# Performance work log

Measured on AMD Instinct MI355X. Metric: run time of the kernel, lower is better.

## Reference

```python
import jax, jax.numpy as jnp
import numpy as np


def setup_inputs() -> dict:
    key = jax.random.key(0)
    inputs = jax.random.normal(key, (4, 1024, 64), dtype=jnp.float32)
    return {"inputs": inputs}


def reference(inputs):
    # inputs: (B, N, D)
    # scores[b,i,j] = sum_d tanh(x[b,i,d] + x[b,j,d])
    addition = inputs[:, :, None, :] + inputs[:, None, :, :]  # (B, N, N, D)
    e_values = jnp.tanh(addition).sum(axis=-1)                # (B, N, N)
    weights = jax.nn.softmax(e_values, axis=-1)               # (B, N, N)
    out = jnp.einsum("bij,bjd->bid", weights, inputs)         # (B, N, D)
    return out
```

## Files before the change

### kernel.cpp

```cpp
#include <hip/hip_runtime.h>


#define NB 4
#define NN 1024
#define ND 64
#define TJ 64
#define NWAVES 4
#define NTILES (NN / TJ)

#if __has_builtin(__builtin_amdgcn_exp2f)
#define EXP2F(x) __builtin_amdgcn_exp2f(x)
#else
#define EXP2F(x) exp2f(x)
#endif
#if __has_builtin(__builtin_amdgcn_rcpf)
#define RCPF(x) __builtin_amdgcn_rcpf(x)
#else
#define RCPF(x) (1.0f / (x))
#endif

static constexpr float C_SCALE = 2.8853900817779268f;

__device__ __forceinline__ float readlane_f(float v, int l) {
    return __uint_as_float(__builtin_amdgcn_readlane(__float_as_uint(v), l));
}

__global__ __launch_bounds__(256) void prep_kernel(const float* __restrict__ x,
                                                   float* __restrict__ E) {
    int idx = blockIdx.x * 256 + threadIdx.x;
    float4 v = ((const float4*)x)[idx];
    float4 e;
    e.x = EXP2F(C_SCALE * v.x);
    e.y = EXP2F(C_SCALE * v.y);
    e.z = EXP2F(C_SCALE * v.z);
    e.w = EXP2F(C_SCALE * v.w);
    ((float4*)E)[idx] = e;
}

template <bool HAS_E>
__global__ __launch_bounds__(256) void addattn_kernel(const float* __restrict__ x,
                                                      const float* __restrict__ E,
                                                      float* __restrict__ out) {
    __shared__ float x_lds[TJ * ND];
    __shared__ float E_lds[TJ * ND];
    __shared__ float Ei_lds[NWAVES * ND];

    const int tid   = threadIdx.x;
    const int lane  = tid & 63;
    const int wave  = tid >> 6;
    const int wg    = blockIdx.x;
    const int b     = wg >> 8;
    const int ibase = (wg & 255) * NWAVES;

    const float* xb = x + (size_t)b * NN * ND;
    const float* Eb = E + (size_t)b * NN * ND;

    Ei_lds[tid] = EXP2F(C_SCALE * xb[(size_t)ibase * ND + tid]);

    float acc    = 0.0f;
    float denomp = 0.0f;

    for (int t = 0; t < NTILES; ++t) {
        __syncthreads();
        {
            const float4* srcx = (const float4*)(xb + (size_t)t * TJ * ND);
            const float4* srcE = (const float4*)(Eb + (size_t)t * TJ * ND);
            #pragma unroll
            for (int it = 0; it < (TJ * ND / 4) / 256; ++it) {
                int idx = it * 256 + tid;
                int j   = idx >> 4;
                int d4  = idx & 15;
                float4 xv = srcx[idx];
                ((float4*)x_lds)[idx] = xv;
                float4 ev;
                if (HAS_E) {
                    ev = srcE[idx];
                } else {
                    ev.x = EXP2F(C_SCALE * xv.x);
                    ev.y = EXP2F(C_SCALE * xv.y);
                    ev.z = EXP2F(C_SCALE * xv.z);
                    ev.w = EXP2F(C_SCALE * xv.w);
                }
                *(float4*)&E_lds[j * ND + ((d4 ^ (j & 15)) << 2)] = ev;
            }
        }
        __syncthreads();

        const int xorkey = lane & 15;
        const float* Eirow = &Ei_lds[wave * ND];
        float rs0 = 0.f, rs1 = 0.f, rs2 = 0.f, rs3 = 0.f;
        #pragma unroll
        for (int d4 = 0; d4 < 16; ++d4) {
            float4 ej = *(const float4*)&E_lds[lane * ND + ((d4 ^ xorkey) << 2)];
            float4 ei = *(const float4*)&Eirow[d4 * 4];
            rs0 += RCPF(fmaf(ei.x, ej.x, 1.0f));
            rs1 += RCPF(fmaf(ei.y, ej.y, 1.0f));
            rs2 += RCPF(fmaf(ei.z, ej.z, 1.0f));
            rs3 += RCPF(fmaf(ei.w, ej.w, 1.0f));
        }
        float rsum = (rs0 + rs1) + (rs2 + rs3);
        float w = EXP2F(-C_SCALE * rsum);
        denomp += w;

        #pragma unroll
        for (int j = 0; j < TJ; ++j) {
            float wj = readlane_f(w, j);
            acc = fmaf(wj, x_lds[j * ND + lane], acc);
        }
    }

    #pragma unroll
    for (int s = 0; s < 6; ++s) denomp += __shfl_xor(denomp, 1 << s, 64);

    const int i = ibase + wave;
    out[((size_t)b * NN + i) * ND + lane] = acc * RCPF(denomp);
}

extern "C" void kernel_launch(void* const* d_in, const int* in_sizes, int n_in,
                              void* d_out, int out_size, void* d_ws, size_t ws_size,
                              hipStream_t stream) {
    const float* x = (const float*)d_in[0];
    float* out = (float*)d_out;
    const size_t e_bytes = (size_t)NB * NN * ND * sizeof(float);

    dim3 grid(NB * (NN / NWAVES));
    dim3 block(256);

    if (ws_size >= e_bytes) {
        float* E = (float*)d_ws;
        prep_kernel<<<dim3(NB * NN * ND / 4 / 256), dim3(256), 0, stream>>>(x, E);
        addattn_kernel<true><<<grid, block, 0, stream>>>(x, E, out);
    } else {
        addattn_kernel<false><<<grid, block, 0, stream>>>(x, (const float*)nullptr, out);
    }
}
```

Before: 74.98 us.

## Process two query rows per wave and stage softmax weights through LDS

Each wave now handles two query rows instead of one, so every key E tile and x tile read from LDS is reused twice, and the grid shrinks to 128 blocks per batch. The per-lane readlane broadcast in the weighted sum is replaced by writing weights to LDS and reading them back as float4, with split accumulators for more instruction-level parallelism. A constant shift is added to the exp2 argument to keep the weights in range. The trade-offs are more registers per thread, fewer total workgroups, and extra LDS traffic for the weights.

```diff
diff --git a/kernel.cpp b/kernel.cpp
--- a/kernel.cpp
+++ b/kernel.cpp
@@ -5,7 +5,8 @@
 #define NN 1024
 #define ND 64
 #define TJ 64
-#define NWAVES 4
+#define TI 8
+#define IPW 2
 #define NTILES (NN / TJ)
 
 #if __has_builtin(__builtin_amdgcn_exp2f)
@@ -20,10 +21,7 @@
 #endif
 
 static constexpr float C_SCALE = 2.8853900817779268f;
-
-__device__ __forceinline__ float readlane_f(float v, int l) {
-    return __uint_as_float(__builtin_amdgcn_readlane(__float_as_uint(v), l));
-}
+static constexpr float K_SHIFT = 46.166241308446828f;
 
 __global__ __launch_bounds__(256) void prep_kernel(const float* __restrict__ x,
                                                    float* __restrict__ E) {
@@ -41,24 +39,37 @@
 __global__ __launch_bounds__(256) void addattn_kernel(const float* __restrict__ x,
                                                       const float* __restrict__ E,
                                                       float* __restrict__ out) {
+    __shared__ float E_lds[TJ * ND];
     __shared__ float x_lds[TJ * ND];
-    __shared__ float E_lds[TJ * ND];
-    __shared__ float Ei_lds[NWAVES * ND];
+    __shared__ float Ei_lds[TI * ND];
+    __shared__ float w_lds[4 * IPW * ND];
 
     const int tid   = threadIdx.x;
     const int lane  = tid & 63;
     const int wave  = tid >> 6;
     const int wg    = blockIdx.x;
-    const int b     = wg >> 8;
-    const int ibase = (wg & 255) * NWAVES;
+    const int b     = wg >> 7;
+    const int ibase = (wg & 127) * TI;
 
     const float* xb = x + (size_t)b * NN * ND;
     const float* Eb = E + (size_t)b * NN * ND;
 
-    Ei_lds[tid] = EXP2F(C_SCALE * xb[(size_t)ibase * ND + tid]);
+    if (tid < TI * ND / 4) {
+        if (HAS_E) {
+            ((float4*)Ei_lds)[tid] = ((const float4*)(Eb + (size_t)ibase * ND))[tid];
+        } else {
+            float4 v = ((const float4*)(xb + (size_t)ibase * ND))[tid];
+            float4 e;
+            e.x = EXP2F(C_SCALE * v.x);
+            e.y = EXP2F(C_SCALE * v.y);
+            e.z = EXP2F(C_SCALE * v.z);
+            e.w = EXP2F(C_SCALE * v.w);
+            ((float4*)Ei_lds)[tid] = e;
+        }
+    }
 
-    float acc    = 0.0f;
-    float denomp = 0.0f;
+    float acc0a = 0.f, acc0b = 0.f, acc1a = 0.f, acc1b = 0.f;
+    float dn0 = 0.f, dn1 = 0.f;
 
     for (int t = 0; t < NTILES; ++t) {
         __syncthreads();
@@ -69,7 +80,7 @@
             for (int it = 0; it < (TJ * ND / 4) / 256; ++it) {
                 int idx = it * 256 + tid;
                 int j   = idx >> 4;
-                int d4  = idx & 15;
+                int c   = idx & 15;
                 float4 xv = srcx[idx];
                 ((float4*)x_lds)[idx] = xv;
                 float4 ev;
@@ -81,39 +92,88 @@
                     ev.z = EXP2F(C_SCALE * xv.z);
                     ev.w = EXP2F(C_SCALE * xv.w);
                 }
-                *(float4*)&E_lds[j * ND + ((d4 ^ (j & 15)) << 2)] = ev;
+                *(float4*)&E_lds[j * ND + ((c ^ (j & 15)) << 2)] = ev;
             }
         }
         __syncthreads();
 
         const int xorkey = lane & 15;
-        const float* Eirow = &Ei_lds[wave * ND];
-        float rs0 = 0.f, rs1 = 0.f, rs2 = 0.f, rs3 = 0.f;
+        const float* Ei0 = &Ei_lds[(wave * IPW + 0) * ND];
+        const float* Ei1 = &Ei_lds[(wave * IPW + 1) * ND];
+        float4 rs0 = {0.f, 0.f, 0.f, 0.f};
+        float4 rs1 = {0.f, 0.f, 0.f, 0.f};
         #pragma unroll
-        for (int d4 = 0; d4 < 16; ++d4) {
-            float4 ej = *(const float4*)&E_lds[lane * ND + ((d4 ^ xorkey) << 2)];
-            float4 ei = *(const float4*)&Eirow[d4 * 4];
-            rs0 += RCPF(fmaf(ei.x, ej.x, 1.0f));
-            rs1 += RCPF(fmaf(ei.y, ej.y, 1.0f));
-            rs2 += RCPF(fmaf(ei.z, ej.z, 1.0f));
-            rs3 += RCPF(fmaf(ei.w, ej.w, 1.0f));
+        for (int c = 0; c < 16; ++c) {
+            float4 ej = *(const float4*)&E_lds[lane * ND + ((c ^ xorkey) << 2)];
+            float4 e0 = *(const float4*)&Ei0[c * 4];
+            float4 e1 = *(const float4*)&Ei1[c * 4];
+            rs0.x += RCPF(fmaf(e0.x, ej.x, 1.0f));
+            rs0.y += RCPF(fmaf(e0.y, ej.y, 1.0f));
+            rs0.z += RCPF(fmaf(e0.z, ej.z, 1.0f));
+            rs0.w += RCPF(fmaf(e0.w, ej.w, 1.0f));
+            rs1.x += RCPF(fmaf(e1.x, ej.x, 1.0f));
+            rs1.y += RCPF(fmaf(e1.y, ej.y, 1.0f));
+            rs1.z += RCPF(fmaf(e1.z, ej.z, 1.0f));
+            rs1.w += RCPF(fmaf(e1.w, ej.w, 1.0f));
         }
-        float rsum = (rs0 + rs1) + (rs2 + rs3);
-        float w = EXP2F(-C_SCALE * rsum);
-        denomp += w;
+        float r0 = (rs0.x + rs0.y) + (rs0.z + rs0.w);
+        float r1 = (rs1.x + rs1.y) + (rs1.z + rs1.w);
+        float w0 = EXP2F(fmaf(-C_SCALE, r0, K_SHIFT));
+        float w1 = EXP2F(fmaf(-C_SCALE, r1, K_SHIFT));
+        dn0 += w0;
+        dn1 += w1;
+
+        w_lds[(wave * IPW + 0) * ND + lane] = w0;
+        w_lds[(wave * IPW + 1) * ND + lane] = w1;
 
         #pragma unroll
-        for (int j = 0; j < TJ; ++j) {
-            float wj = readlane_f(w, j);
-            acc = fmaf(wj, x_lds[j * ND + lane], acc);
+        for (int j8 = 0; j8 < 8; ++j8) {
+            {
+                const int j4 = j8 * 2;
+                float4 wq0 = *(const float4*)&w_lds[(wave * IPW + 0) * ND + j4 * 4];
+                float4 wq1 = *(const float4*)&w_lds[(wave * IPW + 1) * ND + j4 * 4];
+                float xv0 = x_lds[(j4 * 4 + 0) * ND + lane];
+                float xv1 = x_lds[(j4 * 4 + 1) * ND + lane];
+                float xv2 = x_lds[(j4 * 4 + 2) * ND + lane];
+                float xv3 = x_lds[(j4 * 4 + 3) * ND + lane];
+                acc0a = fmaf(wq0.x, xv0, acc0a);
+                acc0a = fmaf(wq0.y, xv1, acc0a);
+                acc0a = fmaf(wq0.z, xv2, acc0a);
+                acc0a = fmaf(wq0.w, xv3, acc0a);
+                acc1a = fmaf(wq1.x, xv0, acc1a);
+                acc1a = fmaf(wq1.y, xv1, acc1a);
+                acc1a = fmaf(wq1.z, xv2, acc1a);
+                acc1a = fmaf(wq1.w, xv3, acc1a);
+            }
+            {
+                const int j4 = j8 * 2 + 1;
+                float4 wq0 = *(const float4*)&w_lds[(wave * IPW + 0) * ND + j4 * 4];
+                float4 wq1 = *(const float4*)&w_lds[(wave * IPW + 1) * ND + j4 * 4];
+                float xv0 = x_lds[(j4 * 4 + 0) * ND + lane];
+                float xv1 = x_lds[(j4 * 4 + 1) * ND + lane];
+                float xv2 = x_lds[(j4 * 4 + 2) * ND + lane];
+                float xv3 = x_lds[(j4 * 4 + 3) * ND + lane];
+                acc0b = fmaf(wq0.x, xv0, acc0b);
+                acc0b = fmaf(wq0.y, xv1, acc0b);
+                acc0b = fmaf(wq0.z, xv2, acc0b);
+                acc0b = fmaf(wq0.w, xv3, acc0b);
+                acc1b = fmaf(wq1.x, xv0, acc1b);
+                acc1b = fmaf(wq1.y, xv1, acc1b);
+                acc1b = fmaf(wq1.z, xv2, acc1b);
+                acc1b = fmaf(wq1.w, xv3, acc1b);
+            }
         }
     }
 
     #pragma unroll
-    for (int s = 0; s < 6; ++s) denomp += __shfl_xor(denomp, 1 << s, 64);
+    for (int s = 0; s < 6; ++s) {
+        dn0 += __shfl_xor(dn0, 1 << s, 64);
+        dn1 += __shfl_xor(dn1, 1 << s, 64);
+    }
 
-    const int i = ibase + wave;
-    out[((size_t)b * NN + i) * ND + lane] = acc * RCPF(denomp);
+    const int i0 = ibase + wave * IPW;
+    out[((size_t)b * NN + i0) * ND + lane]     = (acc0a + acc0b) * RCPF(dn0);
+    out[((size_t)b * NN + i0 + 1) * ND + lane] = (acc1a + acc1b) * RCPF(dn1);
 }
 
 extern "C" void kernel_launch(void* const* d_in, const int* in_sizes, int n_in,
@@ -123,7 +183,7 @@
     float* out = (float*)d_out;
     const size_t e_bytes = (size_t)NB * NN * ND * sizeof(float);
 
-    dim3 grid(NB * (NN / NWAVES));
+    dim3 grid(NB * (NN / TI));
     dim3 block(256);
 
     if (ws_size >= e_bytes) {
```

Measured after the change: 70.92 us. -5.4%, faster.

## Pair tanh reciprocals algebraically and accumulate output per-lane with packed FMAs

Applied to the files above, without the earlier changes.

Combines two reciprocal terms per pair of dimensions into one rcp via the identity 1/(1+a)+1/(1+q) = (2+a+q)/(1+a+q+aq). This halves the transcendental count and uses packed v2f FMAs. The weighted sum over j becomes a per-lane accumulation of 64 output dims in registers, followed by a butterfly transpose-reduction at the end, replacing 64 readlanes per tile. It also reads Ei from global/registers instead of LDS, swizzles x_lds, adds a constant shift to the exponent, and raises the occupancy hint. The trade-offs are much higher register pressure and a costly final shuffle reduction.

```diff
diff --git a/kernel.cpp b/kernel.cpp
--- a/kernel.cpp
+++ b/kernel.cpp
@@ -5,7 +5,7 @@
 #define NN 1024
 #define ND 64
 #define TJ 64
-#define NWAVES 4
+#define TI 4
 #define NTILES (NN / TJ)
 
 #if __has_builtin(__builtin_amdgcn_exp2f)
@@ -20,10 +20,14 @@
 #endif
 
 static constexpr float C_SCALE = 2.8853900817779268f;
+static constexpr float K_SHIFT = 46.166241308446828f;
 
-__device__ __forceinline__ float readlane_f(float v, int l) {
-    return __uint_as_float(__builtin_amdgcn_readlane(__float_as_uint(v), l));
-}
+typedef float v2f __attribute__((ext_vector_type(2)));
+
+#define PKFMA(a, b, c) __builtin_elementwise_fma((a), (b), (c))
+
+__device__ __forceinline__ v2f vlo(float4 v) { v2f r; r.x = v.x; r.y = v.y; return r; }
+__device__ __forceinline__ v2f vhi(float4 v) { v2f r; r.x = v.z; r.y = v.w; return r; }
 
 __global__ __launch_bounds__(256) void prep_kernel(const float* __restrict__ x,
                                                    float* __restrict__ E) {
@@ -38,27 +42,43 @@
 }
 
 template <bool HAS_E>
-__global__ __launch_bounds__(256) void addattn_kernel(const float* __restrict__ x,
-                                                      const float* __restrict__ E,
-                                                      float* __restrict__ out) {
+__global__ __launch_bounds__(256, 3) void addattn_kernel(const float* __restrict__ x,
+                                                         const float* __restrict__ E,
+                                                         float* __restrict__ out) {
+    __shared__ float E_lds[TJ * ND];
     __shared__ float x_lds[TJ * ND];
-    __shared__ float E_lds[TJ * ND];
-    __shared__ float Ei_lds[NWAVES * ND];
 
     const int tid   = threadIdx.x;
     const int lane  = tid & 63;
     const int wave  = tid >> 6;
     const int wg    = blockIdx.x;
     const int b     = wg >> 8;
-    const int ibase = (wg & 255) * NWAVES;
+    const int ibase = (wg & 255) * TI;
+    const int i0    = __builtin_amdgcn_readfirstlane(ibase + wave);
 
-    const float* xb = x + (size_t)b * NN * ND;
-    const float* Eb = E + (size_t)b * NN * ND;
+    const float* xb  = x + (size_t)b * NN * ND;
+    const float* Eb  = E + (size_t)b * NN * ND;
+    const float* Eip = Eb + (size_t)i0 * ND;
 
-    Ei_lds[tid] = EXP2F(C_SCALE * xb[(size_t)ibase * ND + tid]);
+    v2f ei2[32];
+    if (!HAS_E) {
+        #pragma unroll
+        for (int c = 0; c < 16; ++c) {
+            float4 xiq = *(const float4*)&xb[(size_t)i0 * ND + c * 4];
+            v2f lo, hi;
+            lo.x = EXP2F(C_SCALE * xiq.x);
+            lo.y = EXP2F(C_SCALE * xiq.y);
+            hi.x = EXP2F(C_SCALE * xiq.z);
+            hi.y = EXP2F(C_SCALE * xiq.w);
+            ei2[2 * c] = lo;
+            ei2[2 * c + 1] = hi;
+        }
+    }
 
-    float acc    = 0.0f;
-    float denomp = 0.0f;
+    v2f acc2[32];
+    #pragma unroll
+    for (int k = 0; k < 32; ++k) acc2[k] = (v2f){0.f, 0.f};
+    float dn = 0.f;
 
     for (int t = 0; t < NTILES; ++t) {
         __syncthreads();
@@ -69,9 +89,10 @@
             for (int it = 0; it < (TJ * ND / 4) / 256; ++it) {
                 int idx = it * 256 + tid;
                 int j   = idx >> 4;
-                int d4  = idx & 15;
+                int c   = idx & 15;
+                int w   = j * ND + ((c ^ (j & 15)) << 2);
                 float4 xv = srcx[idx];
-                ((float4*)x_lds)[idx] = xv;
+                *(float4*)&x_lds[w] = xv;
                 float4 ev;
                 if (HAS_E) {
                     ev = srcE[idx];
@@ -81,39 +102,62 @@
                     ev.z = EXP2F(C_SCALE * xv.z);
                     ev.w = EXP2F(C_SCALE * xv.w);
                 }
-                *(float4*)&E_lds[j * ND + ((d4 ^ (j & 15)) << 2)] = ev;
+                *(float4*)&E_lds[w] = ev;
             }
         }
         __syncthreads();
 
-        const int xorkey = lane & 15;
-        const float* Eirow = &Ei_lds[wave * ND];
-        float rs0 = 0.f, rs1 = 0.f, rs2 = 0.f, rs3 = 0.f;
+        const int key = lane & 15;
+        v2f rse = {0.f, 0.f}, rso = {0.f, 0.f};
         #pragma unroll
-        for (int d4 = 0; d4 < 16; ++d4) {
-            float4 ej = *(const float4*)&E_lds[lane * ND + ((d4 ^ xorkey) << 2)];
-            float4 ei = *(const float4*)&Eirow[d4 * 4];
-            rs0 += RCPF(fmaf(ei.x, ej.x, 1.0f));
-            rs1 += RCPF(fmaf(ei.y, ej.y, 1.0f));
-            rs2 += RCPF(fmaf(ei.z, ej.z, 1.0f));
-            rs3 += RCPF(fmaf(ei.w, ej.w, 1.0f));
+        for (int c = 0; c < 16; ++c) {
+            float4 ejq = *(const float4*)&E_lds[lane * ND + ((c ^ key) << 2)];
+            v2f eil, eih;
+            if (HAS_E) {
+                float4 eiq = *(const float4*)&Eip[c * 4];
+                eil = vlo(eiq); eih = vhi(eiq);
+            } else {
+                eil = ei2[2 * c]; eih = ei2[2 * c + 1];
+            }
+            v2f a = eil * vlo(ejq);
+            v2f q = eih * vhi(ejq);
+            v2f p = a + q;
+            v2f r = PKFMA(a, q, p + 1.0f);
+            v2f tt; tt.x = RCPF(r.x); tt.y = RCPF(r.y);
+            if (c & 1) rso = PKFMA(p + 2.0f, tt, rso);
+            else       rse = PKFMA(p + 2.0f, tt, rse);
         }
-        float rsum = (rs0 + rs1) + (rs2 + rs3);
-        float w = EXP2F(-C_SCALE * rsum);
-        denomp += w;
+        v2f rs = rse + rso;
+        float rsum = rs.x + rs.y;
+        float w = EXP2F(fmaf(-C_SCALE, rsum, K_SHIFT));
+        dn += w;
+        v2f w2; w2.x = w; w2.y = w;
 
         #pragma unroll
-        for (int j = 0; j < TJ; ++j) {
-            float wj = readlane_f(w, j);
-            acc = fmaf(wj, x_lds[j * ND + lane], acc);
+        for (int c = 0; c < 16; ++c) {
+            float4 xq = *(const float4*)&x_lds[lane * ND + ((c ^ key) << 2)];
+            acc2[2 * c]     = PKFMA(w2, vlo(xq), acc2[2 * c]);
+            acc2[2 * c + 1] = PKFMA(w2, vhi(xq), acc2[2 * c + 1]);
         }
     }
 
+    float* accf = (float*)acc2;
     #pragma unroll
-    for (int s = 0; s < 6; ++s) denomp += __shfl_xor(denomp, 1 << s, 64);
+    for (int s = 0; s < 6; ++s) {
+        const int half = 32 >> s;
+        const int sel  = (lane >> (5 - s)) & 1;
+        #pragma unroll
+        for (int k = 0; k < half; ++k) {
+            float keep = sel ? accf[k + half] : accf[k];
+            float send = sel ? accf[k] : accf[k + half];
+            float recv = __shfl_xor(send, half, 64);
+            accf[k] = keep + recv;
+        }
+    }
+    #pragma unroll
+    for (int s = 0; s < 6; ++s) dn += __shfl_xor(dn, 1 << s, 64);
 
-    const int i = ibase + wave;
-    out[((size_t)b * NN + i) * ND + lane] = acc * RCPF(denomp);
+    out[((size_t)b * NN + i0) * ND + lane] = accf[0] * RCPF(dn);
 }
 
 extern "C" void kernel_launch(void* const* d_in, const int* in_sizes, int n_in,
@@ -123,7 +167,7 @@
     float* out = (float*)d_out;
     const size_t e_bytes = (size_t)NB * NN * ND * sizeof(float);
 
-    dim3 grid(NB * (NN / NWAVES));
+    dim3 grid(NB * (NN / TI));
     dim3 block(256);
 
     if (ws_size >= e_bytes) {
```

Result: faster. 65.24 us (-13.0%).
